# Optimization experiments

Hardware: AMD Instinct MI355X
Metric: run time of the kernel (lower is better)

Reference implementation:

```python
import jax, jax.numpy as jnp
import numpy as np

LN_EPS = 1e-5
W_EPS = 1e-6


def setup_inputs() -> dict:
    key = jax.random.key(0)
    ks = jax.random.split(key, 6)
    B, M, N, D, K = 2, 32768, 4096, 128, 8
    grid_coords = jax.random.uniform(ks[0], (B, M, 3), dtype=jnp.float32)
    point_coords = jax.random.uniform(ks[1], (B, N, 3), dtype=jnp.float32)
    point_feats = jax.random.normal(ks[2], (B, N, D), dtype=jnp.float32)
    # kernel_mlp params: Linear(3,D) -> GELU -> Linear(D,D)
    W1 = jax.random.normal(ks[3], (3, D), dtype=jnp.float32) * 0.1
    b1 = jnp.zeros((D,), dtype=jnp.float32)
    W2 = jax.random.normal(ks[4], (D, D), dtype=jnp.float32) * 0.05
    b2 = jnp.zeros((D,), dtype=jnp.float32)
    gamma = jnp.ones((D,), dtype=jnp.float32)
    beta = jnp.zeros((D,), dtype=jnp.float32)
    return {"grid_coords": grid_coords, "point_coords": point_coords,
            "point_feats": point_feats, "W1": W1, "b1": b1, "W2": W2,
            "b2": b2, "gamma": gamma, "beta": beta, "k": K}


def _gather(src, idx):
    # src: (B,N,C), idx: (B,M,K) -> (B,M,K,C)
    return jax.vmap(lambda s, i: s[i])(src, idx)


def reference(grid_coords, point_coords, point_feats, W1, b1, W2, b2, gamma, beta, k):
    # pairwise euclidean distances (B,M,N), equivalent to torch.cdist
    d2 = (jnp.sum(grid_coords ** 2, -1)[:, :, None]
          + jnp.sum(point_coords ** 2, -1)[:, None, :]
          - 2.0 * jnp.einsum('bmc,bnc->bmn', grid_coords, point_coords))
    dist = jnp.sqrt(jnp.maximum(d2, 0.0))
    # k smallest distances == k largest of -dist
    neg_d, idx = jax.lax.top_k(-dist, k)           # (B,M,K)
    dist_topk = -neg_d
    knn_coords = _gather(point_coords, idx)        # (B,M,K,3)
    knn_feats = _gather(point_feats, idx)          # (B,M,K,D)
    rel_pos = grid_coords[:, :, None, :] - knn_coords
    # kernel MLP (exact GELU, matching nn.GELU default)
    h = jax.nn.gelu(rel_pos @ W1 + b1, approximate=False)
    kappa = h @ W2 + b2                            # (B,M,K,D)
    # inverse-distance weights, normalized over K
    w = 1.0 / (dist_topk + W_EPS)
    w = w / jnp.sum(w, axis=-1, keepdims=True)
    out = jnp.sum(kappa * knn_feats * w[..., None], axis=2)  # (B,M,D)
    # LayerNorm over last dim
    mu = jnp.mean(out, axis=-1, keepdims=True)
    var = jnp.mean((out - mu) ** 2, axis=-1, keepdims=True)
    return (out - mu) * jax.lax.rsqrt(var + LN_EPS) * gamma + beta
```

## Files before the change

### kernel.cpp

```cpp
#include <hip/hip_runtime.h>
#include <math.h>

#define B_ 2
#define M_ 32768
#define N_ 4096
#define D_ 128
#define K_ 8
#define G_ 16
#define NC_ 4096
#define CW_ 0.0625f
#define CAP_ 224

typedef _Float16 half4_t __attribute__((ext_vector_type(4)));
typedef float f32x4 __attribute__((ext_vector_type(4)));
typedef unsigned long long u64;

__device__ __forceinline__ void lex64_insert(u64 k, u64* kd)
{
    if (k < kd[7]) {
        kd[7] = k;
#pragma unroll
        for (int u = 6; u >= 0; --u) {
            if (kd[u+1] < kd[u]) { u64 t = kd[u]; kd[u] = kd[u+1]; kd[u+1] = t; }
        }
    }
}

__device__ __forceinline__ u64 mk_key(float dist, int idx)
{
    return ((u64)__float_as_uint(dist) << 32) | (unsigned)idx;
}

__device__ __forceinline__ void fold64(u64* kd, int mask)
{
    u64 ok[8];
#pragma unroll
    for (int u = 0; u < 8; ++u) ok[u] = __shfl_xor((long long)kd[u], mask);
#pragma unroll
    for (int u = 0; u < 8; ++u) lex64_insert(ok[u], kd);
}

__global__ __launch_bounds__(256) void prep_zero(int* __restrict__ a, int n)
{
    const int i = blockIdx.x * 256 + threadIdx.x;
    if (i < n) a[i] = 0;
}

__global__ __launch_bounds__(256) void prep_hist(
    const float* __restrict__ xyz, int n_per_b, int* __restrict__ hist)
{
    const int i = blockIdx.x * 256 + threadIdx.x;
    if (i >= B_ * n_per_b) return;
    const int b = i / n_per_b;
    const float x = xyz[i*3+0], y = xyz[i*3+1], z = xyz[i*3+2];
    const int cx = min(G_-1, (int)(x * 16.0f));
    const int cy = min(G_-1, (int)(y * 16.0f));
    const int cz = min(G_-1, (int)(z * 16.0f));
    atomicAdd(&hist[b * NC_ + cz*256 + cy*16 + cx], 1);
}

__global__ __launch_bounds__(1024) void prep_scan(
    const int* __restrict__ hist, int* __restrict__ cstart, int* __restrict__ ccur)
{
    __shared__ int lds[1024];
    const int b = blockIdx.x, t = threadIdx.x;
    int v[4]; int s = 0;
#pragma unroll
    for (int j = 0; j < 4; ++j) { v[j] = hist[b*NC_ + t*4 + j]; s += v[j]; }
    lds[t] = s;
    __syncthreads();
    for (int off = 1; off < 1024; off <<= 1) {
        int x = (t >= off) ? lds[t - off] : 0;
        __syncthreads();
        lds[t] += x;
        __syncthreads();
    }
    int excl = lds[t] - s;
#pragma unroll
    for (int j = 0; j < 4; ++j) {
        cstart[b*(NC_+1) + t*4 + j] = excl;
        ccur[b*NC_ + t*4 + j] = excl;
        excl += v[j];
    }
    if (t == 1023) cstart[b*(NC_+1) + NC_] = excl;
}

__global__ __launch_bounds__(256) void prep_scatter_p(
    const float* __restrict__ pts, int* __restrict__ ccur,
    float4* __restrict__ p4s, int* __restrict__ sidx)
{
#pragma clang fp contract(off)
    const int i = blockIdx.x * 256 + threadIdx.x;
    if (i >= B_ * N_) return;
    const int b = i >> 12, loc = i & (N_-1);
    const float x = pts[i*3+0], y = pts[i*3+1], z = pts[i*3+2];
    const int cx = min(G_-1, (int)(x * 16.0f));
    const int cy = min(G_-1, (int)(y * 16.0f));
    const int cz = min(G_-1, (int)(z * 16.0f));
    const int pos = atomicAdd(&ccur[b*NC_ + cz*256 + cy*16 + cx], 1);
    float4 v; v.x = x; v.y = y; v.z = z;
    v.w = (z * z + y * y) + x * x;
    p4s[b*N_ + pos] = v;
    sidx[b*N_ + pos] = loc;
}

__global__ __launch_bounds__(256) void prep_scatter_q(
    const float* __restrict__ grid_c, int* __restrict__ qcur,
    float4* __restrict__ q4s, int* __restrict__ qmap)
{
#pragma clang fp contract(off)
    const int i = blockIdx.x * 256 + threadIdx.x;
    if (i >= B_ * M_) return;
    const int b = i >> 15;
    const float x = grid_c[i*3+0], y = grid_c[i*3+1], z = grid_c[i*3+2];
    const int cx = min(G_-1, (int)(x * 16.0f));
    const int cy = min(G_-1, (int)(y * 16.0f));
    const int cz = min(G_-1, (int)(z * 16.0f));
    const int pos = atomicAdd(&qcur[b*NC_ + cz*256 + cy*16 + cx], 1);
    float4 v; v.x = x; v.y = y; v.z = z;
    v.w = (z * z + y * y) + x * x;
    q4s[(size_t)b*M_ + pos] = v;
    qmap[(size_t)b*M_ + pos] = i;
}

__global__ __launch_bounds__(256) void prep_w2t(
    const float* __restrict__ W2, _Float16* __restrict__ w2t_hi)
{
    const int i = blockIdx.x * 256 + threadIdx.x;
    if (i >= D_ * D_) return;
    const int n = i >> 7, k = i & 127;
    w2t_hi[i] = (_Float16)W2[k * D_ + n];
}

__global__ __launch_bounds__(256) void knn_kernel(
    const float4* __restrict__ q4s, const int* __restrict__ qmap,
    const float4* __restrict__ p4s, const int* __restrict__ sidx,
    const int* __restrict__ cstart, const int* __restrict__ qstart,
    int* __restrict__ out_idx, float* __restrict__ out_w)
{
#pragma clang fp contract(off)
    __shared__ float4 spt[4][CAP_];
    __shared__ int    sil[4][CAP_];
    __shared__ int    rtab[4][32][2];

    const int tid  = threadIdx.x;
    const int wv   = tid >> 6;
    const int lane = tid & 63;
    const int gci  = blockIdx.x * 4 + wv;
    const int b    = gci >> 12;
    const int cid  = gci & (NC_ - 1);
    const int cx = cid & 15, cy = (cid >> 4) & 15, cz = cid >> 8;

    const int* __restrict__ cs = cstart + b * (NC_ + 1);
    const int qs0 = qstart[b * (NC_ + 1) + cid];
    const int nq  = qstart[b * (NC_ + 1) + cid + 1] - qs0;

    const float4* p4 = p4s + (size_t)b * N_;
    const int*    sx = sidx + (size_t)b * N_;

    const int z0 = max(0, cz-2), z1 = min(G_-1, cz+2);
    const int y0 = max(0, cy-2), y1 = min(G_-1, cy+2);
    const int x0 = max(0, cx-2), x1 = min(G_-1, cx+2);
    const int ny = y1 - y0 + 1;
    const int nrows = (z1 - z0 + 1) * ny;

    int myS = 0, myLen = 0;
    if (nq > 0 && lane < nrows) {
        const int zz = z0 + lane / ny;
        const int yy = y0 + lane % ny;
        const int cb = zz*256 + yy*16;
        myS   = cs[cb + x0];
        myLen = cs[cb + x1 + 1] - myS;
    }
    int inc = myLen;
#pragma unroll
    for (int o = 1; o < 64; o <<= 1) {
        int v = __shfl_up(inc, o);
        if (lane >= o) inc += v;
    }
    const int off = inc - myLen;
    const int tot = __shfl(inc, 63);
    const bool ovf = (tot > CAP_);
    if (nq > 0 && lane < nrows) {
        rtab[wv][lane][0] = myS;
        rtab[wv][lane][1] = myLen;
        if (!ovf) {
            for (int t = 0; t < myLen; ++t) {
                spt[wv][off + t] = p4[myS + t];
                sil[wv][off + t] = sx[myS + t];
            }
        }
    }
    __syncthreads();

    const int qg  = lane >> 2;
    const int sub = lane & 3;

    for (int q0 = 0; q0 < nq; q0 += 16) {
        const bool act = (q0 + qg) < nq;
        float gx = 0.f, gy = 0.f, gz = 0.f, sg2 = 0.f;
        int qorig = 0;
        if (act) {
            const size_t slot = (size_t)b * M_ + qs0 + q0 + qg;
            const float4 qv = q4s[slot];
            gx = qv.x; gy = qv.y; gz = qv.z; sg2 = qv.w;
            qorig = qmap[slot];
        }

        u64 kd[8];
#pragma unroll
        for (int u = 0; u < 8; ++u) kd[u] = ~0ull;

        if (act) {
            if (!ovf) {
                const int ts = (sub * tot) >> 2;
                const int te = ((sub + 1) * tot) >> 2;
                for (int t = ts; t < te; ++t) {
                    const float4 pp = spt[wv][t];
                    const float dot  = fmaf(gz, pp.z, fmaf(gy, pp.y, gx * pp.x));
                    const float d2   = fmaf(dot, -2.0f, sg2 + pp.w);
                    const float dist = sqrtf(fmaxf(d2, 0.0f));
                    lex64_insert(mk_key(dist, sil[wv][t]), kd);
                }
            } else {
                const int r0 = (sub * nrows) >> 2;
                const int r1 = ((sub + 1) * nrows) >> 2;
                for (int r = r0; r < r1; ++r) {
                    const int gs = rtab[wv][r][0];
                    const int ln = rtab[wv][r][1];
                    for (int t = 0; t < ln; ++t) {
                        const float4 pp = p4[gs + t];
                        const float dot  = fmaf(gz, pp.z, fmaf(gy, pp.y, gx * pp.x));
                        const float d2   = fmaf(dot, -2.0f, sg2 + pp.w);
                        const float dist = sqrtf(fmaxf(d2, 0.0f));
                        lex64_insert(mk_key(dist, sx[gs + t]), kd);
                    }
                }
            }
        }
        fold64(kd, 1);
        fold64(kd, 2);

        int R = 2;
        while (R < G_ - 1) {
            const float bd7 = __uint_as_float((unsigned)(kd[7] >> 32));
            const bool need = act && !(bd7 < (float)R * CW_ - 1e-5f);
            if (!__any(need)) break;
            ++R;
            if (need) {
                u64 fk[8];
#pragma unroll
                for (int u = 0; u < 8; ++u) fk[u] = ~0ull;
                int m2 = 0;
                for (int zz = cz - R; zz <= cz + R; ++zz) {
                    if (zz < 0 || zz > G_-1) continue;
                    for (int yy = cy - R; yy <= cy + R; ++yy) {
                        if (yy < 0 || yy > G_-1) continue;
                        const int ch = max(abs(zz - cz), abs(yy - cy));
                        if (((m2++) & 3) != sub) continue;
                        const int cb = zz*256 + yy*16;
                        int s0, e0, s1 = 0, e1 = 0;
                        if (ch == R) {
                            s0 = cs[cb + max(0, cx-R)];
                            e0 = cs[cb + min(G_-1, cx+R) + 1];
                        } else {
                            const int xl = cx - R, xr = cx + R;
                            s0 = (xl >= 0)    ? cs[cb+xl]   : 0;
                            e0 = (xl >= 0)    ? cs[cb+xl+1] : 0;
                            s1 = (xr <= G_-1) ? cs[cb+xr]   : 0;
                            e1 = (xr <= G_-1) ? cs[cb+xr+1] : 0;
                        }
                        for (int t = s0; t < e0; ++t) {
                            const float4 pp = p4[t];
                            const float dot  = fmaf(gz, pp.z, fmaf(gy, pp.y, gx * pp.x));
                            const float d2   = fmaf(dot, -2.0f, sg2 + pp.w);
                            const float dist = sqrtf(fmaxf(d2, 0.0f));
                            lex64_insert(mk_key(dist, sx[t]), fk);
                        }
                        for (int t = s1; t < e1; ++t) {
                            const float4 pp = p4[t];
                            const float dot  = fmaf(gz, pp.z, fmaf(gy, pp.y, gx * pp.x));
                            const float d2   = fmaf(dot, -2.0f, sg2 + pp.w);
                            const float dist = sqrtf(fmaxf(d2, 0.0f));
                            lex64_insert(mk_key(dist, sx[t]), fk);
                        }
                    }
                }
                fold64(fk, 1);
                fold64(fk, 2);
#pragma unroll
                for (int u = 0; u < 8; ++u) lex64_insert(fk[u], kd);
            }
        }

        if (act && sub == 0) {
            float wk8[8];
#pragma unroll
            for (int u = 0; u < 8; ++u) {
                const float dist = __uint_as_float((unsigned)(kd[u] >> 32));
                wk8[u] = 1.0f / (dist + 1e-6f);
            }
            float wsum = wk8[0];
#pragma unroll
            for (int u = 1; u < 8; ++u) wsum = wsum + wk8[u];
            const float winv = 1.0f / wsum;
#pragma unroll
            for (int u = 0; u < 8; ++u) {
                out_idx[qorig * 8 + u] = (int)(kd[u] & 0xffffffffu);
                out_w[qorig * 8 + u]   = wk8[u] * winv;
            }
        }
    }
}

__device__ __forceinline__ float gelu_f(float u)
{
    const float t  = u * 0.70710678118654752f;
    const float t2 = t * t;
    float p = fmaf(t2, 1.0f/9360.0f, -1.0f/1320.0f);
    p = fmaf(t2, p, 1.0f/216.0f);
    p = fmaf(t2, p, -1.0f/42.0f);
    p = fmaf(t2, p, 1.0f/10.0f);
    p = fmaf(t2, p, -1.0f/3.0f);
    p = fmaf(t2, p, 1.0f);
    float er = 1.1283791670955126f * t * p;
    if (fabsf(t) > 0.5f) er = erff(t);
    return 0.5f * u * (1.0f + er);
}

#define HSTR 132
__global__ __launch_bounds__(256) void gno_kernel(
    const float* __restrict__ grid_c, const float* __restrict__ pts,
    const float* __restrict__ feats,
    const float* __restrict__ W1, const float* __restrict__ b1,
    const _Float16* __restrict__ w2t_hi,
    const float* __restrict__ b2,
    const float* __restrict__ gmm, const float* __restrict__ bta,
    const int* __restrict__ kidx, const float* __restrict__ kw,
    float* __restrict__ out)
{
    __shared__ __align__(16) _Float16 smem_h[64][HSTR];
    _Float16 (*kappa)[HSTR] = (_Float16(*)[HSTR])&smem_h[0][0];
    __shared__ float srel[8][8][4];
    __shared__ float swt[8][8];
    __shared__ int   sid[8][8];

    const int tid = threadIdx.x;
    const int qb8 = blockIdx.x * 8;

    if (tid < 64) {
        const int qq = tid >> 3, k = tid & 7;
        const int gq = qb8 + qq;
        const int id = kidx[gq * 8 + k];
        sid[qq][k] = id;
        swt[qq][k] = kw[gq * 8 + k];
        const int bb = gq >> 15;
        const float* pp = pts + ((size_t)bb * N_ + id) * 3;
        srel[qq][k][0] = grid_c[gq * 3 + 0] - pp[0];
        srel[qq][k][1] = grid_c[gq * 3 + 1] - pp[1];
        srel[qq][k][2] = grid_c[gq * 3 + 2] - pp[2];
    }

    const int qs = tid >> 5;
    const int dg = tid & 31;

    const float4 w1r0 = *(const float4*)(W1 + dg * 4);
    const float4 w1r1 = *(const float4*)(W1 + D_ + dg * 4);
    const float4 w1r2 = *(const float4*)(W1 + 2 * D_ + dg * 4);
    const float4 w1bb = *(const float4*)(b1 + dg * 4);
    __syncthreads();

#pragma unroll
    for (int k = 0; k < 8; ++k) {
        const float rx = srel[qs][k][0];
        const float ry = srel[qs][k][1];
        const float rz = srel[qs][k][2];
        half4_t hv;
        hv[0] = (_Float16)gelu_f(rx * w1r0.x + ry * w1r1.x + rz * w1r2.x + w1bb.x);
        hv[1] = (_Float16)gelu_f(rx * w1r0.y + ry * w1r1.y + rz * w1r2.y + w1bb.y);
        hv[2] = (_Float16)gelu_f(rx * w1r0.z + ry * w1r1.z + rz * w1r2.z + w1bb.z);
        hv[3] = (_Float16)gelu_f(rx * w1r0.w + ry * w1r1.w + rz * w1r2.w + w1bb.w);
        *(half4_t*)&smem_h[qs * 8 + k][dg * 4] = hv;
    }
    __syncthreads();

    const int wv   = tid >> 6;
    const int lane = tid & 63;
    const int mrow = lane & 15;
    const int kq   = lane >> 4;

    f32x4 acc[4][2];
#pragma unroll
    for (int mt = 0; mt < 4; ++mt)
#pragma unroll
        for (int ntl = 0; ntl < 2; ++ntl)
            acc[mt][ntl] = (f32x4){0.f, 0.f, 0.f, 0.f};

#pragma unroll
    for (int ntl = 0; ntl < 2; ++ntl) {
        const int n = (wv * 2 + ntl) * 16 + mrow;
        half4_t Bh[8];
#pragma unroll
        for (int ks = 0; ks < 8; ++ks)
            Bh[ks] = *(const half4_t*)(w2t_hi + n * D_ + ks * 16 + kq * 4);
#pragma unroll
        for (int mt = 0; mt < 4; ++mt) {
            const int row = mt * 16 + mrow;
#pragma unroll
            for (int ks = 0; ks < 8; ++ks) {
                const half4_t Ah = *(const half4_t*)&smem_h[row][ks * 16 + kq * 4];
                acc[mt][ntl] = __builtin_amdgcn_mfma_f32_16x16x16f16(
                    Ah, Bh[ks], acc[mt][ntl], 0, 0, 0);
            }
        }
    }
    __syncthreads();

#pragma unroll
    for (int mt = 0; mt < 4; ++mt)
#pragma unroll
        for (int ntl = 0; ntl < 2; ++ntl) {
            const int col = (wv * 2 + ntl) * 16 + mrow;
#pragma unroll
            for (int r = 0; r < 4; ++r)
                kappa[mt * 16 + kq * 4 + r][col] = (_Float16)acc[mt][ntl][r];
        }
    __syncthreads();

    const int gq = qb8 + qs;
    const int bb = gq >> 15;
    const float4 b2v = *(const float4*)(b2 + dg * 4);

    float o0 = 0.0f, o1 = 0.0f, o2 = 0.0f, o3 = 0.0f;
#pragma unroll
    for (int k = 0; k < 8; ++k) {
        const half4_t kp = *(const half4_t*)&kappa[qs * 8 + k][dg * 4];
        const float4 f =
            *(const float4*)(feats + ((size_t)bb * N_ + sid[qs][k]) * D_ + dg * 4);
        const float wk = swt[qs][k];
        o0 += wk * f.x * ((float)kp[0] + b2v.x);
        o1 += wk * f.y * ((float)kp[1] + b2v.y);
        o2 += wk * f.z * ((float)kp[2] + b2v.z);
        o3 += wk * f.w * ((float)kp[3] + b2v.w);
    }

    float s = o0 + o1 + o2 + o3;
#pragma unroll
    for (int off = 16; off > 0; off >>= 1) s += __shfl_xor(s, off, 32);
    const float mu = s * (1.0f / 128.0f);
    const float v0 = o0 - mu, v1 = o1 - mu, v2 = o2 - mu, v3 = o3 - mu;
    float vs = v0 * v0 + v1 * v1 + v2 * v2 + v3 * v3;
#pragma unroll
    for (int off = 16; off > 0; off >>= 1) vs += __shfl_xor(vs, off, 32);
    const float inv = 1.0f / sqrtf(vs * (1.0f / 128.0f) + 1e-5f);

    const float4 gv = *(const float4*)(gmm + dg * 4);
    const float4 bv = *(const float4*)(bta + dg * 4);
    float4 ov;
    ov.x = v0 * inv * gv.x + bv.x;
    ov.y = v1 * inv * gv.y + bv.y;
    ov.z = v2 * inv * gv.z + bv.z;
    ov.w = v3 * inv * gv.w + bv.w;
    *(float4*)(out + (size_t)gq * D_ + dg * 4) = ov;
}

extern "C" void kernel_launch(void* const* d_in, const int* in_sizes, int n_in,
                              void* d_out, int out_size, void* d_ws, size_t ws_size,
                              hipStream_t stream)
{
    (void)in_sizes; (void)n_in; (void)out_size; (void)ws_size;
    const float* grid_c = (const float*)d_in[0];
    const float* pts    = (const float*)d_in[1];
    const float* feats  = (const float*)d_in[2];
    const float* W1     = (const float*)d_in[3];
    const float* b1     = (const float*)d_in[4];
    const float* W2     = (const float*)d_in[5];
    const float* b2     = (const float*)d_in[6];
    const float* gmm    = (const float*)d_in[7];
    const float* bta    = (const float*)d_in[8];
    float* out = (float*)d_out;

    char* w = (char*)d_ws;
    int*    kidx   = (int*)(w);
    float*  kw     = (float*)(w + 2097152);
    float4* p4s    = (float4*)(w + 4194304);
    float4* q4s    = (float4*)(w + 4325376);
    int*    sidx   = (int*)(w + 5373952);
    int*    qmap   = (int*)(w + 5406720);
    int*    cstart = (int*)(w + 5668864);
    int*    qstart = (int*)(w + 5701640);
    int*    ccur   = (int*)(w + 5734416);
    int*    qcur   = (int*)(w + 5767184);
    int*    hist   = (int*)(w + 5799952);
    int*    qhist  = (int*)(w + 5832720);
    _Float16* w2t_hi = (_Float16*)(w + 5865488);

    prep_zero<<<(2 * B_ * NC_ + 255) / 256, 256, 0, stream>>>(hist, 2 * B_ * NC_);
    prep_hist<<<(B_ * N_ + 255) / 256, 256, 0, stream>>>(pts, N_, hist);
    prep_hist<<<(B_ * M_ + 255) / 256, 256, 0, stream>>>(grid_c, M_, qhist);
    prep_w2t<<<(D_ * D_ + 255) / 256, 256, 0, stream>>>(W2, w2t_hi);
    prep_scan<<<B_, 1024, 0, stream>>>(hist, cstart, ccur);
    prep_scan<<<B_, 1024, 0, stream>>>(qhist, qstart, qcur);
    prep_scatter_p<<<(B_ * N_ + 255) / 256, 256, 0, stream>>>(pts, ccur, p4s, sidx);
    prep_scatter_q<<<(B_ * M_ + 255) / 256, 256, 0, stream>>>(grid_c, qcur, q4s, qmap);
    knn_kernel<<<(B_ * NC_) / 4, 256, 0, stream>>>(q4s, qmap, p4s, sidx, cstart,
                                                   qstart, kidx, kw);
    gno_kernel<<<(B_ * M_) / 8, 256, 0, stream>>>(grid_c, pts, feats, W1, b1,
                                                  w2t_hi, b2, gmm, bta,
                                                  kidx, kw, out);
}
```

Measured before the change: 205.0 us.

## Merge preprocessing kernels and compute GELU polynomial in packed fp16

```diff
diff --git a/kernel.cpp b/kernel.cpp
--- a/kernel.cpp
+++ b/kernel.cpp
@@ -40,96 +40,95 @@
     for (int u = 0; u < 8; ++u) lex64_insert(ok[u], kd);
 }
 
-__global__ __launch_bounds__(256) void prep_zero(int* __restrict__ a, int n)
+__global__ __launch_bounds__(256) void prep_hist_all(
+    const float* __restrict__ pts, const float* __restrict__ grid_c,
+    int* __restrict__ hist)
 {
     const int i = blockIdx.x * 256 + threadIdx.x;
-    if (i < n) a[i] = 0;
-}
-
-__global__ __launch_bounds__(256) void prep_hist(
-    const float* __restrict__ xyz, int n_per_b, int* __restrict__ hist)
-{
-    const int i = blockIdx.x * 256 + threadIdx.x;
-    if (i >= B_ * n_per_b) return;
-    const int b = i / n_per_b;
-    const float x = xyz[i*3+0], y = xyz[i*3+1], z = xyz[i*3+2];
-    const int cx = min(G_-1, (int)(x * 16.0f));
-    const int cy = min(G_-1, (int)(y * 16.0f));
-    const int cz = min(G_-1, (int)(z * 16.0f));
-    atomicAdd(&hist[b * NC_ + cz*256 + cy*16 + cx], 1);
-}
-
-__global__ __launch_bounds__(1024) void prep_scan(
+    const int NP = B_ * N_;
+    if (i < NP) {
+        const float x = pts[i*3+0], y = pts[i*3+1], z = pts[i*3+2];
+        const int cx = min(G_-1, (int)(x * 16.0f));
+        const int cy = min(G_-1, (int)(y * 16.0f));
+        const int cz = min(G_-1, (int)(z * 16.0f));
+        atomicAdd(&hist[(i >> 12) * NC_ + cz*256 + cy*16 + cx], 1);
+    } else if (i < NP + B_ * M_) {
+        const int j = i - NP;
+        const float x = grid_c[j*3+0], y = grid_c[j*3+1], z = grid_c[j*3+2];
+        const int cx = min(G_-1, (int)(x * 16.0f));
+        const int cy = min(G_-1, (int)(y * 16.0f));
+        const int cz = min(G_-1, (int)(z * 16.0f));
+        atomicAdd(&hist[(B_ + (j >> 15)) * NC_ + cz*256 + cy*16 + cx], 1);
+    }
+}
+
+__global__ __launch_bounds__(256) void prep_scan(
     const int* __restrict__ hist, int* __restrict__ cstart, int* __restrict__ ccur)
 {
-    __shared__ int lds[1024];
+    __shared__ int wsum[4];
     const int b = blockIdx.x, t = threadIdx.x;
-    int v[4]; int s = 0;
-#pragma unroll
-    for (int j = 0; j < 4; ++j) { v[j] = hist[b*NC_ + t*4 + j]; s += v[j]; }
-    lds[t] = s;
+    const int lane = t & 63, wv = t >> 6;
+    int v[16]; int s = 0;
+#pragma unroll
+    for (int j = 0; j < 16; ++j) { v[j] = hist[b*NC_ + t*16 + j]; s += v[j]; }
+    int inc = s;
+#pragma unroll
+    for (int o = 1; o < 64; o <<= 1) {
+        int x = __shfl_up(inc, o);
+        if (lane >= o) inc += x;
+    }
+    if (lane == 63) wsum[wv] = inc;
     __syncthreads();
-    for (int off = 1; off < 1024; off <<= 1) {
-        int x = (t >= off) ? lds[t - off] : 0;
-        __syncthreads();
-        lds[t] += x;
-        __syncthreads();
-    }
-    int excl = lds[t] - s;
-#pragma unroll
-    for (int j = 0; j < 4; ++j) {
-        cstart[b*(NC_+1) + t*4 + j] = excl;
-        ccur[b*NC_ + t*4 + j] = excl;
+    int woff = 0;
+    for (int w2 = 0; w2 < wv; ++w2) woff += wsum[w2];
+    int excl = woff + inc - s;
+#pragma unroll
+    for (int j = 0; j < 16; ++j) {
+        cstart[b*(NC_+1) + t*16 + j] = excl;
+        ccur[b*NC_ + t*16 + j] = excl;
         excl += v[j];
     }
-    if (t == 1023) cstart[b*(NC_+1) + NC_] = excl;
-}
-
-__global__ __launch_bounds__(256) void prep_scatter_p(
-    const float* __restrict__ pts, int* __restrict__ ccur,
-    float4* __restrict__ p4s, int* __restrict__ sidx)
+    if (t == 255) cstart[b*(NC_+1) + NC_] = excl;
+}
+
+__global__ __launch_bounds__(256) void prep_scatter_all(
+    const float* __restrict__ pts, const float* __restrict__ grid_c,
+    const float* __restrict__ W2, int* __restrict__ ccur,
+    float4* __restrict__ p4s, int* __restrict__ sidx,
+    float4* __restrict__ q4s, int* __restrict__ qmap,
+    _Float16* __restrict__ w2t_hi)
 {
 #pragma clang fp contract(off)
     const int i = blockIdx.x * 256 + threadIdx.x;
-    if (i >= B_ * N_) return;
-    const int b = i >> 12, loc = i & (N_-1);
-    const float x = pts[i*3+0], y = pts[i*3+1], z = pts[i*3+2];
-    const int cx = min(G_-1, (int)(x * 16.0f));
-    const int cy = min(G_-1, (int)(y * 16.0f));
-    const int cz = min(G_-1, (int)(z * 16.0f));
-    const int pos = atomicAdd(&ccur[b*NC_ + cz*256 + cy*16 + cx], 1);
-    float4 v; v.x = x; v.y = y; v.z = z;
-    v.w = (z * z + y * y) + x * x;
-    p4s[b*N_ + pos] = v;
-    sidx[b*N_ + pos] = loc;
-}
-
-__global__ __launch_bounds__(256) void prep_scatter_q(
-    const float* __restrict__ grid_c, int* __restrict__ qcur,
-    float4* __restrict__ q4s, int* __restrict__ qmap)
-{
-#pragma clang fp contract(off)
-    const int i = blockIdx.x * 256 + threadIdx.x;
-    if (i >= B_ * M_) return;
-    const int b = i >> 15;
-    const float x = grid_c[i*3+0], y = grid_c[i*3+1], z = grid_c[i*3+2];
-    const int cx = min(G_-1, (int)(x * 16.0f));
-    const int cy = min(G_-1, (int)(y * 16.0f));
-    const int cz = min(G_-1, (int)(z * 16.0f));
-    const int pos = atomicAdd(&qcur[b*NC_ + cz*256 + cy*16 + cx], 1);
-    float4 v; v.x = x; v.y = y; v.z = z;
-    v.w = (z * z + y * y) + x * x;
-    q4s[(size_t)b*M_ + pos] = v;
-    qmap[(size_t)b*M_ + pos] = i;
-}
-
-__global__ __launch_bounds__(256) void prep_w2t(
-    const float* __restrict__ W2, _Float16* __restrict__ w2t_hi)
-{
-    const int i = blockIdx.x * 256 + threadIdx.x;
-    if (i >= D_ * D_) return;
-    const int n = i >> 7, k = i & 127;
-    w2t_hi[i] = (_Float16)W2[k * D_ + n];
+    const int NP = B_ * N_, NQ = B_ * M_;
+    if (i < NP) {
+        const int b = i >> 12, loc = i & (N_-1);
+        const float x = pts[i*3+0], y = pts[i*3+1], z = pts[i*3+2];
+        const int cx = min(G_-1, (int)(x * 16.0f));
+        const int cy = min(G_-1, (int)(y * 16.0f));
+        const int cz = min(G_-1, (int)(z * 16.0f));
+        const int pos = atomicAdd(&ccur[b*NC_ + cz*256 + cy*16 + cx], 1);
+        float4 v; v.x = x; v.y = y; v.z = z;
+        v.w = (z * z + y * y) + x * x;
+        p4s[b*N_ + pos] = v;
+        sidx[b*N_ + pos] = loc;
+    } else if (i < NP + NQ) {
+        const int j = i - NP;
+        const int b = j >> 15;
+        const float x = grid_c[j*3+0], y = grid_c[j*3+1], z = grid_c[j*3+2];
+        const int cx = min(G_-1, (int)(x * 16.0f));
+        const int cy = min(G_-1, (int)(y * 16.0f));
+        const int cz = min(G_-1, (int)(z * 16.0f));
+        const int pos = atomicAdd(&ccur[(B_ + b)*NC_ + cz*256 + cy*16 + cx], 1);
+        float4 v; v.x = x; v.y = y; v.z = z;
+        v.w = (z * z + y * y) + x * x;
+        q4s[(size_t)b*M_ + pos] = v;
+        qmap[(size_t)b*M_ + pos] = j;
+    } else if (i < NP + NQ + D_ * D_) {
+        const int m = i - NP - NQ;
+        const int n = m >> 7, k = m & 127;
+        w2t_hi[m] = (_Float16)W2[k * D_ + n];
+    }
 }
 
 __global__ __launch_bounds__(256) void knn_kernel(
@@ -313,21 +312,6 @@
     }
 }
 
-__device__ __forceinline__ float gelu_f(float u)
-{
-    const float t  = u * 0.70710678118654752f;
-    const float t2 = t * t;
-    float p = fmaf(t2, 1.0f/9360.0f, -1.0f/1320.0f);
-    p = fmaf(t2, p, 1.0f/216.0f);
-    p = fmaf(t2, p, -1.0f/42.0f);
-    p = fmaf(t2, p, 1.0f/10.0f);
-    p = fmaf(t2, p, -1.0f/3.0f);
-    p = fmaf(t2, p, 1.0f);
-    float er = 1.1283791670955126f * t * p;
-    if (fabsf(t) > 0.5f) er = erff(t);
-    return 0.5f * u * (1.0f + er);
-}
-
 #define HSTR 132
 __global__ __launch_bounds__(256) void gno_kernel(
     const float* __restrict__ grid_c, const float* __restrict__ pts,
@@ -375,11 +359,27 @@
         const float rx = srel[qs][k][0];
         const float ry = srel[qs][k][1];
         const float rz = srel[qs][k][2];
-        half4_t hv;
-        hv[0] = (_Float16)gelu_f(rx * w1r0.x + ry * w1r1.x + rz * w1r2.x + w1bb.x);
-        hv[1] = (_Float16)gelu_f(rx * w1r0.y + ry * w1r1.y + rz * w1r2.y + w1bb.y);
-        hv[2] = (_Float16)gelu_f(rx * w1r0.z + ry * w1r1.z + rz * w1r2.z + w1bb.z);
-        hv[3] = (_Float16)gelu_f(rx * w1r0.w + ry * w1r1.w + rz * w1r2.w + w1bb.w);
+        const float u0 = rx * w1r0.x + ry * w1r1.x + rz * w1r2.x + w1bb.x;
+        const float u1 = rx * w1r0.y + ry * w1r1.y + rz * w1r2.y + w1bb.y;
+        const float u2 = rx * w1r0.z + ry * w1r1.z + rz * w1r2.z + w1bb.z;
+        const float u3 = rx * w1r0.w + ry * w1r1.w + rz * w1r2.w + w1bb.w;
+        half4_t uh;
+        uh[0] = (_Float16)u0; uh[1] = (_Float16)u1;
+        uh[2] = (_Float16)u2; uh[3] = (_Float16)u3;
+        const half4_t t  = uh * (_Float16)0.70710678118654752f;
+        const half4_t t2 = t * t;
+        half4_t p = t2 * (_Float16)0.1f + (_Float16)(-1.0f/3.0f);
+        p = t2 * p + (_Float16)1.0f;
+        const half4_t er = (t * p) * (_Float16)1.1283791670955126f;
+        half4_t hv = (uh * (_Float16)0.5f) * (er + (_Float16)1.0f);
+        const float am = fmaxf(fmaxf(fabsf(u0), fabsf(u1)),
+                               fmaxf(fabsf(u2), fabsf(u3)));
+        if (am > 0.5f) {
+            hv[0] = (_Float16)(0.5f*u0*(1.0f+erff(u0*0.70710678118654752f)));
+            hv[1] = (_Float16)(0.5f*u1*(1.0f+erff(u1*0.70710678118654752f)));
+            hv[2] = (_Float16)(0.5f*u2*(1.0f+erff(u2*0.70710678118654752f)));
+            hv[3] = (_Float16)(0.5f*u3*(1.0f+erff(u3*0.70710678118654752f)));
+        }
         *(half4_t*)&smem_h[qs * 8 + k][dg * 4] = hv;
     }
     __syncthreads();
@@ -494,15 +494,14 @@
     int*    hist   = (int*)(w + 5799952);
     int*    qhist  = (int*)(w + 5832720);
     _Float16* w2t_hi = (_Float16*)(w + 5865488);
-
-    prep_zero<<<(2 * B_ * NC_ + 255) / 256, 256, 0, stream>>>(hist, 2 * B_ * NC_);
-    prep_hist<<<(B_ * N_ + 255) / 256, 256, 0, stream>>>(pts, N_, hist);
-    prep_hist<<<(B_ * M_ + 255) / 256, 256, 0, stream>>>(grid_c, M_, qhist);
-    prep_w2t<<<(D_ * D_ + 255) / 256, 256, 0, stream>>>(W2, w2t_hi);
-    prep_scan<<<B_, 1024, 0, stream>>>(hist, cstart, ccur);
-    prep_scan<<<B_, 1024, 0, stream>>>(qhist, qstart, qcur);
-    prep_scatter_p<<<(B_ * N_ + 255) / 256, 256, 0, stream>>>(pts, ccur, p4s, sidx);
-    prep_scatter_q<<<(B_ * M_ + 255) / 256, 256, 0, stream>>>(grid_c, qcur, q4s, qmap);
+    (void)qhist; (void)qcur;
+
+    hipMemsetAsync(hist, 0, (size_t)2 * B_ * NC_ * sizeof(int), stream);
+    prep_hist_all<<<(B_ * (N_ + M_) + 255) / 256, 256, 0, stream>>>(
+        pts, grid_c, hist);
+    prep_scan<<<2 * B_, 256, 0, stream>>>(hist, cstart, ccur);
+    prep_scatter_all<<<(B_ * (N_ + M_) + D_ * D_ + 255) / 256, 256, 0, stream>>>(
+        pts, grid_c, W2, ccur, p4s, sidx, q4s, qmap, w2t_hi);
     knn_kernel<<<(B_ * NC_) / 4, 256, 0, stream>>>(q4s, qmap, p4s, sidx, cstart,
                                                    qstart, kidx, kw);
     gno_kernel<<<(B_ * M_) / 8, 256, 0, stream>>>(grid_c, pts, feats, W1, b1,
```

Measured after the change: 193.2 us. 5.8% less time.
